# Optimization experiments

Hardware: AMD Instinct MI355X
Metric: run time of the kernel (lower is better)

The kernel has to match this reference:

```python
import jax, jax.numpy as jnp
from jax import lax
import numpy as np

B, L, D, F, T, NB = 32, 512, 256, 256, 2048, 256
LN_EPS = 1e-5


def _layer_norm(h, g, b):
    m = jnp.mean(h, axis=-1, keepdims=True)
    v = jnp.mean((h - m) ** 2, axis=-1, keepdims=True)
    return (h - m) * lax.rsqrt(v + LN_EPS) * g + b


def _predictor(h, prm):
    # Conv1d(k=3, pad=1) -> ReLU -> LayerNorm, twice, then Linear(F->1) -> ReLU -> squeeze
    # (dropout is identity in this deterministic reference)
    c1w, c1b, g1, b1, c2w, c2b, g2, b2, lw, lb = prm
    h = lax.conv_general_dilated(h, c1w, (1,), 'SAME', dimension_numbers=('NWC', 'WIO', 'NWC')) + c1b
    h = _layer_norm(jax.nn.relu(h), g1, b1)
    h = lax.conv_general_dilated(h, c2w, (1,), 'SAME', dimension_numbers=('NWC', 'WIO', 'NWC')) + c2b
    h = _layer_norm(jax.nn.relu(h), g2, b2)
    return jax.nn.relu(jnp.einsum('btf,f->bt', h, lw) + lb)  # [B, T]


def _length_regulate(x, dur, t_out):
    # Gather-based equivalent of the dense alignment-matrix matmul in LengthRegulator.LR:
    # frame t maps to phoneme j with cum[j-1] <= t < cum[j]; frames past total duration are zero.
    cum = jnp.cumsum(dur, axis=1)                                          # [B, L]
    t = jnp.arange(t_out)                                                  # [T]
    idx = jax.vmap(lambda c: jnp.searchsorted(c, t, side='right'))(cum)    # [B, T]
    valid = idx < dur.shape[1]
    idx = jnp.clip(idx, 0, dur.shape[1] - 1)
    out = jnp.take_along_axis(x, idx[..., None], axis=1)                   # [B, T, D]
    return jnp.where(valid[..., None], out, jnp.zeros((), x.dtype))


def setup_inputs() -> dict:
    key = jax.random.key(0)
    ks = iter(jax.random.split(key, 64))

    def nrm(shape, s=0.05):
        return jax.random.normal(next(ks), shape, jnp.float32) * s

    inp = dict(
        x=jax.random.normal(next(ks), (B, L, D), jnp.float32),
        d_target=jax.random.randint(next(ks), (B, L), 0, 4, jnp.int32),
        e_target=jax.random.normal(next(ks), (B, T), jnp.float32),
        p_target=jax.random.normal(next(ks), (B, T), jnp.float32),
        mel_max_length=T,
    )
    for p in ('dur', 'en', 'pi'):
        inp[p + '_c1w'] = nrm((3, D, F)); inp[p + '_c1b'] = jnp.zeros((F,), jnp.float32)
        inp[p + '_g1'] = jnp.ones((F,), jnp.float32); inp[p + '_b1'] = jnp.zeros((F,), jnp.float32)
        inp[p + '_c2w'] = nrm((3, F, F)); inp[p + '_c2b'] = jnp.zeros((F,), jnp.float32)
        inp[p + '_g2'] = jnp.ones((F,), jnp.float32); inp[p + '_b2'] = jnp.zeros((F,), jnp.float32)
        inp[p + '_lw'] = nrm((F,)); inp[p + '_lb'] = jnp.zeros((), jnp.float32)
    inp['en_emb'] = nrm((NB, D), 0.1)
    inp['pi_emb'] = nrm((NB, D), 0.1)
    inp['en_bins'] = jnp.linspace(-3.0, 3.0, NB - 1, dtype=jnp.float32)
    inp['pi_bins'] = jnp.linspace(-3.0, 3.0, NB - 1, dtype=jnp.float32)
    return inp


def reference(x, d_target, e_target, p_target, mel_max_length,
              dur_c1w, dur_c1b, dur_g1, dur_b1, dur_c2w, dur_c2b, dur_g2, dur_b2, dur_lw, dur_lb,
              en_c1w, en_c1b, en_g1, en_b1, en_c2w, en_c2b, en_g2, en_b2, en_lw, en_lb,
              pi_c1w, pi_c1b, pi_g1, pi_b1, pi_c2w, pi_c2b, pi_g2, pi_b2, pi_lw, pi_lb,
              en_emb, pi_emb, en_bins, pi_bins):
    dur_prm = (dur_c1w, dur_c1b, dur_g1, dur_b1, dur_c2w, dur_c2b, dur_g2, dur_b2, dur_lw, dur_lb)
    en_prm = (en_c1w, en_c1b, en_g1, en_b1, en_c2w, en_c2b, en_g2, en_b2, en_lw, en_lb)
    pi_prm = (pi_c1w, pi_c1b, pi_g1, pi_b1, pi_c2w, pi_c2b, pi_g2, pi_b2, pi_lw, pi_lb)

    log_dur = _predictor(x, dur_prm)                               # [B, L]
    h = _length_regulate(x, d_target, mel_max_length)              # [B, T, D]

    energy_pred = _predictor(h, en_prm)                            # [B, T]
    e_idx = jnp.searchsorted(en_bins, e_target, side='left')       # torch.bucketize(right=False)
    h = h + jnp.take(en_emb, e_idx, axis=0)

    pitch_pred = _predictor(h, pi_prm)                             # [B, T]
    p_idx = jnp.searchsorted(pi_bins, p_target, side='left')
    h = h + jnp.take(pi_emb, p_idx, axis=0)

    return (h, log_dur, pitch_pred, energy_pred)
```

## Files before the change

### kernel.cpp

```cpp
#include <hip/hip_runtime.h>
#include <hip/hip_bf16.h>
#include <cstddef>

constexpr int B = 32, L = 512, D = 256, F = 256, T = 2048, NB = 256;
constexpr float LN_EPS = 1e-5f;
constexpr int BDIM = 256;
constexpr int WFRAGS = 24 * 16 * 64;

constexpr int N_FH  = 1024;
constexpr int NT_L  = 9;
constexpr int NT_T  = 34;
constexpr int N_DUR = NT_L * B;
constexpr int N_TP  = NT_T * B;

typedef __attribute__((ext_vector_type(8))) short short8;
typedef __attribute__((ext_vector_type(4))) short short4v;
typedef __attribute__((ext_vector_type(4))) float f32x4;

__device__ inline short f2bf(float x) {
    __hip_bfloat16 h = __float2bfloat16(x);
    return __builtin_bit_cast(short, h);
}

__global__ void cumsum_kernel(const int* __restrict__ dt, int* __restrict__ cum) {
    __shared__ int s[L];
    const int b = blockIdx.x, tid = threadIdx.x;
    s[tid] = dt[b * L + tid];
    __syncthreads();
    for (int off = 1; off < L; off <<= 1) {
        int v = (tid >= off) ? s[tid - off] : 0;
        __syncthreads();
        s[tid] += v;
        __syncthreads();
    }
    cum[b * L + tid] = s[tid];
}

__global__ void idx_kernel(const int* __restrict__ cum,
                           const float* __restrict__ et, const float* __restrict__ ebins,
                           const float* __restrict__ pt, const float* __restrict__ pbins,
                           int* __restrict__ gidx, int* __restrict__ eidx, int* __restrict__ pidx) {
    const int r = blockIdx.x * BDIM + threadIdx.x;
    const int b = r >> 11, t = r & (T - 1);
    const int* c = cum + b * L;
    int lo = 0, hi = L;
    while (lo < hi) { const int mid = (lo + hi) >> 1; if (c[mid] <= t) lo = mid + 1; else hi = mid; }
    gidx[r] = (lo < L) ? lo : -1;
    const float e = et[r];
    int el = 0, eh = NB - 1;
    while (el < eh) { const int mid = (el + eh) >> 1; if (ebins[mid] < e) el = mid + 1; else eh = mid; }
    eidx[r] = el;
    const float p = pt[r];
    int pl = 0, ph = NB - 1;
    while (pl < ph) { const int mid = (pl + ph) >> 1; if (pbins[mid] < p) pl = mid + 1; else ph = mid; }
    pidx[r] = pl;
}

__global__ void wprep_kernel(const float* __restrict__ w0, const float* __restrict__ w1,
                             const float* __restrict__ w2, const float* __restrict__ w3,
                             const float* __restrict__ w4, const float* __restrict__ w5,
                             short* __restrict__ wb) {
    const float* ws[6] = {w0, w1, w2, w3, w4, w5};
    const float* w = ws[blockIdx.y];
    short* dst = wb + (size_t)blockIdx.y * WFRAGS * 8;
    const int phi = blockIdx.x * BDIM + threadIdx.x;
    const int kb = phi >> 10;
    const int n16 = (phi >> 6) & 15;
    const int lane = phi & 63;
    const int kconv = kb >> 3, dblk = kb & 7;
    const int kg = lane >> 4;
    const int fcol = (n16 >> 2) * 64 + (lane & 15) * 4 + (n16 & 3);
    const float* src = w + (size_t)kconv * D * F + (dblk * 32 + kg * 8) * F + fcol;
    short8 o;
    #pragma unroll
    for (int j = 0; j < 8; j++) o[j] = f2bf(src[j * F]);
    *(short8*)(dst + (size_t)phi * 8) = o;
}

__global__ void zv_kernel(const float* __restrict__ cb1, const float* __restrict__ g1,
                          const float* __restrict__ b1,
                          const float* __restrict__ w2, const float* __restrict__ cb2,
                          const float* __restrict__ g2, const float* __restrict__ b2,
                          const float* __restrict__ lw, const float* __restrict__ lb,
                          float* __restrict__ zv) {
    __shared__ float z1s[F];
    __shared__ float red[8];
    const int f = threadIdx.x;
    const int wv = f >> 6, lane = f & 63;

    float v = fmaxf(cb1[f], 0.f);
    float s = v, q = v * v;
    #pragma unroll
    for (int msk = 1; msk < 64; msk <<= 1) { s += __shfl_xor(s, msk); q += __shfl_xor(q, msk); }
    if (lane == 0) { red[wv] = s; red[4 + wv] = q; }
    __syncthreads();
    {
        const float S = red[0] + red[1] + red[2] + red[3];
        const float Q = red[4] + red[5] + red[6] + red[7];
        const float m = S * (1.f / 256.f);
        const float var = fmaxf(Q * (1.f / 256.f) - m * m, 0.f);
        const float rs = rsqrtf(var + LN_EPS);
        z1s[f] = (v - m) * rs * g1[f] + b1[f];
    }
    __syncthreads();

    float y = cb2[f];
    for (int d = 0; d < D; d++) {
        y += z1s[d] * (w2[(size_t)d * F + f] + w2[((size_t)D + d) * F + f]
                       + w2[((size_t)2 * D + d) * F + f]);
    }
    v = fmaxf(y, 0.f);
    s = v; q = v * v;
    #pragma unroll
    for (int msk = 1; msk < 64; msk <<= 1) { s += __shfl_xor(s, msk); q += __shfl_xor(q, msk); }
    __syncthreads();
    if (lane == 0) { red[wv] = s; red[4 + wv] = q; }
    __syncthreads();
    const float S = red[0] + red[1] + red[2] + red[3];
    const float Q = red[4] + red[5] + red[6] + red[7];
    const float m = S * (1.f / 256.f);
    const float var = fmaxf(Q * (1.f / 256.f) - m * m, 0.f);
    const float rs = rsqrtf(var + LN_EPS);
    float p = ((v - m) * rs * g2[f] + b2[f]) * lw[f];
    #pragma unroll
    for (int msk = 1; msk < 64; msk <<= 1) p += __shfl_xor(p, msk);
    __syncthreads();
    if (lane == 0) red[wv] = p;
    __syncthreads();
    if (f == 0) zv[0] = fmaxf(red[0] + red[1] + red[2] + red[3] + lb[0], 0.f);
}

__device__ __forceinline__ void conv_mfma16(const short8 (&a)[4], const short8 (&bb)[4],
                                            f32x4 (&acc)[4][4]) {
    __builtin_amdgcn_s_setprio(1);
    #pragma unroll
    for (int m = 0; m < 4; m++)
        #pragma unroll
        for (int n = 0; n < 4; n++)
            acc[m][n] = __builtin_amdgcn_mfma_f32_16x16x32_bf16(a[m], bb[n], acc[m][n], 0, 0, 0);
    __builtin_amdgcn_s_setprio(0);
}

__device__ __forceinline__ void conv_kloop(const short* in_s, const short8* bw,
                                           f32x4 (&acc)[4][4], int w,
                                           int lane, int kg, int lr) {
    const short8* bp = bw + (w * 4) * 64 + lane;
    short8 bA[4], bB[4];
    #pragma unroll
    for (int n = 0; n < 4; n++) bA[n] = bp[n * 64];
    bp += 1024;
    #pragma unroll
    for (int n = 0; n < 4; n++) bB[n] = bp[n * 64];
    bp += 1024;

    #pragma unroll
    for (int kconv = 0; kconv < 3; kconv++) {
        const short* rowp = in_s + (lr + kconv) * 256;
        const int xb = (lr + kconv) & 7;
        #pragma unroll 1
        for (int db = 0; db < 8; db += 2) {
            short8 a[4];
            {
                const short* ab = rowp + (((db * 4 + kg) ^ xb) << 3);
                #pragma unroll
                for (int m = 0; m < 4; m++) a[m] = *(const short8*)(ab + m * 4096);
                conv_mfma16(a, bA, acc);
                #pragma unroll
                for (int n = 0; n < 4; n++) bA[n] = bp[n * 64];
                bp += 1024;
            }
            {
                const short* ab = rowp + ((((db + 1) * 4 + kg) ^ xb) << 3);
                #pragma unroll
                for (int m = 0; m < 4; m++) a[m] = *(const short8*)(ab + m * 4096);
                conv_mfma16(a, bB, acc);
                #pragma unroll
                for (int n = 0; n < 4; n++) bB[n] = bp[n * 64];
                bp += 1024;
            }
        }
    }
}

struct PredParams {
    const short* wb1; const short* wb2;
    const float *cb1, *g1, *b1, *cb2, *g2, *b2, *lw, *lb;
    const int* eidx; const float* emb;
    const float* zv;
    float* out;
    int Tlen;
    int mode;
};

__launch_bounds__(BDIM, 4)
__global__ void mega_kernel(const float* __restrict__ xin,
                            const int* __restrict__ gidx,
                            const int* __restrict__ cum,
                            const int* __restrict__ eidxA,
                            const int* __restrict__ pidxA,
                            const float* __restrict__ eemb,
                            const float* __restrict__ pemb,
                            float* __restrict__ h,
                            PredParams pd, PredParams pe, PredParams pp) {
    __shared__ short in_s[66 * 256];
    __shared__ float red_s[4][64], red_q[4][64];
    __shared__ float row_m[64], row_rs[64];
    __shared__ float dot_p[4][64];

    const int tid = threadIdx.x;
    const int w = tid >> 6, lane = tid & 63;

    int id = blockIdx.x;
    if (id < N_FH) {
        const int row0 = id * 64 + w * 16;
        #pragma unroll 4
        for (int i = 0; i < 16; i++) {
            const int row = row0 + i;
            const int b = row >> 11;
            const int g = gidx[row], ei = eidxA[row], pi = pidxA[row];
            float4 v = make_float4(0.f, 0.f, 0.f, 0.f);
            if (g >= 0) v = *(const float4*)(xin + ((size_t)b * L + g) * D + lane * 4);
            const float4 ev = *(const float4*)(eemb + (size_t)ei * D + lane * 4);
            const float4 pv = *(const float4*)(pemb + (size_t)pi * D + lane * 4);
            v.x += ev.x + pv.x; v.y += ev.y + pv.y; v.z += ev.z + pv.z; v.w += ev.w + pv.w;
            *(float4*)(h + (size_t)row * D + lane * 4) = v;
        }
        return;
    }
    id -= N_FH;

    PredParams P;
    int b, tx;
    if (id < N_DUR) {
        P = pd; b = id / NT_L; tx = id % NT_L;
    } else if (id < N_DUR + N_TP) {
        id -= N_DUR;
        P = pe; b = id / NT_T; tx = id % NT_T;
    } else {
        id -= N_DUR + N_TP;
        P = pp; b = id / NT_T; tx = id % NT_T;
    }
    const int Tlen = P.Tlen;
    const int t0 = tx * 62;
    const int kg = lane >> 4, lr = lane & 15;

    if (P.zv != nullptr) {
        const int ctot = cum[(b + 1) * L - 1];
        if (t0 - 2 >= ctot) {
            if (tid < 62) {
                const int t = t0 + tid;
                if (t < Tlen) P.out[(size_t)b * Tlen + t] = P.zv[0];
            }
            return;
        }
    }

    constexpr int TASKS = 66 * 32;
    constexpr int BATCH = 4;
    const bool has_emb = (P.emb != nullptr);
    for (int base = 0; base < TASKS; base += BATCH * BDIM) {
        float4 fa[BATCH], fb[BATCH], ea[BATCH], eb[BATCH];
        #pragma unroll
        for (int j = 0; j < BATCH; j++) {
            fa[j] = make_float4(0.f, 0.f, 0.f, 0.f); fb[j] = fa[j];
            ea[j] = fa[j]; eb[j] = fa[j];
            const int task = base + j * BDIM + tid;
            if (task < TASKS) {
                const int row = task >> 5, slot = task & 31;
                const int t = t0 - 2 + row;
                if (t >= 0 && t < Tlen) {
                    if (P.mode == 0) {
                        const float* p = xin + ((size_t)b * Tlen + t) * D + slot * 8;
                        fa[j] = *(const float4*)p; fb[j] = *(const float4*)(p + 4);
                    } else {
                        const int g = gidx[b * T + t];
                        if (g >= 0) {
                            const float* p = xin + ((size_t)b * L + g) * D + slot * 8;
                            fa[j] = *(const float4*)p; fb[j] = *(const float4*)(p + 4);
                        }
                        if (has_emb) {
                            const float* er = P.emb + (size_t)P.eidx[b * T + t] * F + slot * 8;
                            ea[j] = *(const float4*)er; eb[j] = *(const float4*)(er + 4);
                        }
                    }
                }
            }
        }
        #pragma unroll
        for (int j = 0; j < BATCH; j++) {
            const int task = base + j * BDIM + tid;
            if (task < TASKS) {
                const int row = task >> 5, slot = task & 31;
                short8 frag;
                frag[0] = f2bf(fa[j].x + ea[j].x); frag[1] = f2bf(fa[j].y + ea[j].y);
                frag[2] = f2bf(fa[j].z + ea[j].z); frag[3] = f2bf(fa[j].w + ea[j].w);
                frag[4] = f2bf(fb[j].x + eb[j].x); frag[5] = f2bf(fb[j].y + eb[j].y);
                frag[6] = f2bf(fb[j].z + eb[j].z); frag[7] = f2bf(fb[j].w + eb[j].w);
                *(short8*)(in_s + row * 256 + ((slot ^ (row & 7)) << 3)) = frag;
            }
        }
    }
    __syncthreads();

    f32x4 acc[4][4];
    #pragma unroll
    for (int m = 0; m < 4; m++)
        #pragma unroll
        for (int n = 0; n < 4; n++)
            acc[m][n] = (f32x4){0.f, 0.f, 0.f, 0.f};
    conv_kloop(in_s, (const short8*)P.wb1, acc, w, lane, kg, lr);

    const int cbase = w * 64 + lr * 4;
    const f32x4 c1v = *(const f32x4*)(P.cb1 + cbase);
    const f32x4 g1v = *(const f32x4*)(P.g1 + cbase);
    const f32x4 b1v = *(const f32x4*)(P.b1 + cbase);

    #pragma unroll
    for (int m = 0; m < 4; m++) {
        #pragma unroll
        for (int reg = 0; reg < 4; reg++) {
            float s = 0.f, q = 0.f;
            #pragma unroll
            for (int n = 0; n < 4; n++) {
                const float v = fmaxf(acc[m][n][reg] + c1v[n], 0.f);
                acc[m][n][reg] = v;
                s += v; q += v * v;
            }
            #pragma unroll
            for (int msk = 1; msk < 16; msk <<= 1) { s += __shfl_xor(s, msk); q += __shfl_xor(q, msk); }
            if (lr == 0) {
                const int r = m * 16 + kg * 4 + reg;
                red_s[w][r] = s; red_q[w][r] = q;
            }
        }
    }
    __syncthreads();
    if (tid < 64) {
        const float s = red_s[0][tid] + red_s[1][tid] + red_s[2][tid] + red_s[3][tid];
        const float q = red_q[0][tid] + red_q[1][tid] + red_q[2][tid] + red_q[3][tid];
        const float mm = s * (1.f / 256.f);
        const float var = fmaxf(q * (1.f / 256.f) - mm * mm, 0.f);
        row_m[tid] = mm;
        row_rs[tid] = rsqrtf(var + LN_EPS);
    }
    if (tid >= 128 && tid < 192) {
        short8 z = {};
        *(short8*)(in_s + 64 * 256 + (tid - 128) * 8) = z;
    }
    __syncthreads();

    #pragma unroll
    for (int m = 0; m < 4; m++) {
        #pragma unroll
        for (int reg = 0; reg < 4; reg++) {
            const int r1 = m * 16 + kg * 4 + reg;
            const int tg = t0 - 1 + r1;
            const bool ok = (tg >= 0) && (tg < Tlen);
            const float mm = row_m[r1], rs = row_rs[r1];
            short4v o;
            #pragma unroll
            for (int n = 0; n < 4; n++) {
                const float v = ok ? (acc[m][n][reg] - mm) * rs * g1v[n] + b1v[n] : 0.f;
                o[n] = f2bf(v);
            }
            *(short4v*)(in_s + r1 * 256 + (((cbase >> 3) ^ (r1 & 7)) << 3) + (cbase & 7)) = o;
        }
    }
    __syncthreads();

    #pragma unroll
    for (int m = 0; m < 4; m++)
        #pragma unroll
        for (int n = 0; n < 4; n++)
            acc[m][n] = (f32x4){0.f, 0.f, 0.f, 0.f};
    conv_kloop(in_s, (const short8*)P.wb2, acc, w, lane, kg, lr);

    const f32x4 c2v = *(const f32x4*)(P.cb2 + cbase);
    const f32x4 g2v = *(const f32x4*)(P.g2 + cbase);
    const f32x4 b2v = *(const f32x4*)(P.b2 + cbase);
    const f32x4 lwv = *(const f32x4*)(P.lw + cbase);

    #pragma unroll
    for (int m = 0; m < 4; m++) {
        #pragma unroll
        for (int reg = 0; reg < 4; reg++) {
            float s = 0.f, q = 0.f;
            #pragma unroll
            for (int n = 0; n < 4; n++) {
                const float v = fmaxf(acc[m][n][reg] + c2v[n], 0.f);
                acc[m][n][reg] = v;
                s += v; q += v * v;
            }
            #pragma unroll
            for (int msk = 1; msk < 16; msk <<= 1) { s += __shfl_xor(s, msk); q += __shfl_xor(q, msk); }
            if (lr == 0) {
                const int r = m * 16 + kg * 4 + reg;
                red_s[w][r] = s; red_q[w][r] = q;
            }
        }
    }
    __syncthreads();
    if (tid < 64) {
        const float s = red_s[0][tid] + red_s[1][tid] + red_s[2][tid] + red_s[3][tid];
        const float q = red_q[0][tid] + red_q[1][tid] + red_q[2][tid] + red_q[3][tid];
        const float mm = s * (1.f / 256.f);
        const float var = fmaxf(q * (1.f / 256.f) - mm * mm, 0.f);
        row_m[tid] = mm;
        row_rs[tid] = rsqrtf(var + LN_EPS);
    }
    __syncthreads();
    #pragma unroll
    for (int m = 0; m < 4; m++) {
        #pragma unroll
        for (int reg = 0; reg < 4; reg++) {
            const int r = m * 16 + kg * 4 + reg;
            const float mm = row_m[r], rs = row_rs[r];
            float p = 0.f;
            #pragma unroll
            for (int n = 0; n < 4; n++)
                p += ((acc[m][n][reg] - mm) * rs * g2v[n] + b2v[n]) * lwv[n];
            #pragma unroll
            for (int msk = 1; msk < 16; msk <<= 1) p += __shfl_xor(p, msk);
            if (lr == 0) dot_p[w][r] = p;
        }
    }
    __syncthreads();
    if (tid < 62) {
        const int t = t0 + tid;
        if (t < Tlen) {
            const float p = dot_p[0][tid] + dot_p[1][tid] + dot_p[2][tid] + dot_p[3][tid] + P.lb[0];
            P.out[(size_t)b * Tlen + t] = fmaxf(p, 0.f);
        }
    }
}

extern "C" void kernel_launch(void* const* d_in, const int* in_sizes, int n_in,
                              void* d_out, int out_size, void* d_ws, size_t ws_size,
                              hipStream_t stream) {
    const float* x        = (const float*)d_in[0];
    const int*   d_target = (const int*)d_in[1];
    const float* e_target = (const float*)d_in[2];
    const float* p_target = (const float*)d_in[3];

    const float* const* P = (const float* const*)d_in;
    const float* en_emb  = (const float*)d_in[35];
    const float* pi_emb  = (const float*)d_in[36];
    const float* en_bins = (const float*)d_in[37];
    const float* pi_bins = (const float*)d_in[38];

    float* out = (float*)d_out;
    float* h        = out;
    float* log_dur  = out + (size_t)B * T * D;
    float* pitch    = log_dur + (size_t)B * L;
    float* energy   = pitch + (size_t)B * T;

    short* wbs  = (short*)d_ws;
    int*   cum  = (int*)(wbs + (size_t)6 * WFRAGS * 8);
    int*   gidx = cum + B * L;
    int*   eidx = gidx + B * T;
    int*   pidx = eidx + B * T;
    float* zvp  = (float*)(pidx + B * T);

    wprep_kernel<<<dim3(WFRAGS / BDIM, 6), BDIM, 0, stream>>>(
        P[5], P[9], P[15], P[19], P[25], P[29], wbs);

    cumsum_kernel<<<B, L, 0, stream>>>(d_target, cum);
    idx_kernel<<<B * T / BDIM, BDIM, 0, stream>>>(
        cum, e_target, en_bins, p_target, pi_bins, gidx, eidx, pidx);

    zv_kernel<<<1, BDIM, 0, stream>>>(
        P[16], P[17], P[18], P[19], P[20], P[21], P[22], P[23], P[24], zvp);

    PredParams dur_p = { wbs + (size_t)0 * WFRAGS * 8, wbs + (size_t)1 * WFRAGS * 8,
                         P[6], P[7], P[8], P[10], P[11], P[12], P[13], P[14],
                         nullptr, nullptr, nullptr, log_dur, L, 0 };
    PredParams en_p  = { wbs + (size_t)2 * WFRAGS * 8, wbs + (size_t)3 * WFRAGS * 8,
                         P[16], P[17], P[18], P[20], P[21], P[22], P[23], P[24],
                         nullptr, nullptr, zvp, energy, T, 1 };
    PredParams pi_p  = { wbs + (size_t)4 * WFRAGS * 8, wbs + (size_t)5 * WFRAGS * 8,
                         P[26], P[27], P[28], P[30], P[31], P[32], P[33], P[34],
                         eidx, en_emb, nullptr, pitch, T, 1 };

    mega_kernel<<<N_FH + N_DUR + 2 * N_TP, BDIM, 0, stream>>>(
        x, gidx, cum, eidx, pidx, en_emb, pi_emb, h, dur_p, en_p, pi_p);
}
```

Measured before the change: 153.1 us.

## Fuse preamble kernels and precompute embedding-conv table for pitch padding tiles

Merges weight prep, cumsum, index search and the constant-output computation into one preamble launch, cutting launch overhead and serial gaps. For pitch-predictor tiles past the total duration (where input is only the energy embedding), it precomputes a table of energy-embedding rows times each first-conv tap. Those tiles then build the first conv output by summing table rows instead of running the first MFMA conv. This adds a 768-block table-building pass and extra workspace, plus a different numeric path (fp32 table, then bf16 round) for those tiles.

```diff
diff --git a/kernel.cpp b/kernel.cpp
--- a/kernel.cpp
+++ b/kernel.cpp
@@ -13,6 +13,11 @@
 constexpr int N_DUR = NT_L * B;
 constexpr int N_TP  = NT_T * B;
 
+constexpr int PRE_WPREP = 576;
+constexpr int PRE_WTAB  = 768;
+constexpr int PRE_IDX   = 32;
+constexpr int PRE_TOTAL = PRE_WPREP + PRE_WTAB + PRE_IDX + 1;
+
 typedef __attribute__((ext_vector_type(8))) short short8;
 typedef __attribute__((ext_vector_type(4))) short short4v;
 typedef __attribute__((ext_vector_type(4))) float f32x4;
@@ -21,113 +26,144 @@
     __hip_bfloat16 h = __float2bfloat16(x);
     return __builtin_bit_cast(short, h);
 }
-
-__global__ void cumsum_kernel(const int* __restrict__ dt, int* __restrict__ cum) {
-    __shared__ int s[L];
-    const int b = blockIdx.x, tid = threadIdx.x;
-    s[tid] = dt[b * L + tid];
-    __syncthreads();
-    for (int off = 1; off < L; off <<= 1) {
-        int v = (tid >= off) ? s[tid - off] : 0;
-        __syncthreads();
-        s[tid] += v;
-        __syncthreads();
-    }
-    cum[b * L + tid] = s[tid];
+__device__ inline float bf2f(short s) {
+    unsigned u = ((unsigned)(unsigned short)s) << 16;
+    return __builtin_bit_cast(float, u);
 }
 
-__global__ void idx_kernel(const int* __restrict__ cum,
-                           const float* __restrict__ et, const float* __restrict__ ebins,
-                           const float* __restrict__ pt, const float* __restrict__ pbins,
-                           int* __restrict__ gidx, int* __restrict__ eidx, int* __restrict__ pidx) {
-    const int r = blockIdx.x * BDIM + threadIdx.x;
-    const int b = r >> 11, t = r & (T - 1);
-    const int* c = cum + b * L;
-    int lo = 0, hi = L;
-    while (lo < hi) { const int mid = (lo + hi) >> 1; if (c[mid] <= t) lo = mid + 1; else hi = mid; }
-    gidx[r] = (lo < L) ? lo : -1;
-    const float e = et[r];
-    int el = 0, eh = NB - 1;
-    while (el < eh) { const int mid = (el + eh) >> 1; if (ebins[mid] < e) el = mid + 1; else eh = mid; }
-    eidx[r] = el;
-    const float p = pt[r];
-    int pl = 0, ph = NB - 1;
-    while (pl < ph) { const int mid = (pl + ph) >> 1; if (pbins[mid] < p) pl = mid + 1; else ph = mid; }
-    pidx[r] = pl;
-}
-
-__global__ void wprep_kernel(const float* __restrict__ w0, const float* __restrict__ w1,
-                             const float* __restrict__ w2, const float* __restrict__ w3,
-                             const float* __restrict__ w4, const float* __restrict__ w5,
-                             short* __restrict__ wb) {
-    const float* ws[6] = {w0, w1, w2, w3, w4, w5};
-    const float* w = ws[blockIdx.y];
-    short* dst = wb + (size_t)blockIdx.y * WFRAGS * 8;
-    const int phi = blockIdx.x * BDIM + threadIdx.x;
-    const int kb = phi >> 10;
-    const int n16 = (phi >> 6) & 15;
-    const int lane = phi & 63;
-    const int kconv = kb >> 3, dblk = kb & 7;
-    const int kg = lane >> 4;
-    const int fcol = (n16 >> 2) * 64 + (lane & 15) * 4 + (n16 & 3);
-    const float* src = w + (size_t)kconv * D * F + (dblk * 32 + kg * 8) * F + fcol;
-    short8 o;
-    #pragma unroll
-    for (int j = 0; j < 8; j++) o[j] = f2bf(src[j * F]);
-    *(short8*)(dst + (size_t)phi * 8) = o;
-}
-
-__global__ void zv_kernel(const float* __restrict__ cb1, const float* __restrict__ g1,
-                          const float* __restrict__ b1,
-                          const float* __restrict__ w2, const float* __restrict__ cb2,
-                          const float* __restrict__ g2, const float* __restrict__ b2,
-                          const float* __restrict__ lw, const float* __restrict__ lb,
-                          float* __restrict__ zv) {
-    __shared__ float z1s[F];
+__global__ void preamble_kernel(const float* __restrict__ w0, const float* __restrict__ w1,
+                                const float* __restrict__ w2, const float* __restrict__ w3,
+                                const float* __restrict__ w4, const float* __restrict__ w5,
+                                const int* __restrict__ dt,
+                                const float* __restrict__ et, const float* __restrict__ ebins,
+                                const float* __restrict__ pt, const float* __restrict__ pbins,
+                                const float* __restrict__ en_emb, const float* __restrict__ pi_c1w,
+                                const float* __restrict__ zcb1, const float* __restrict__ zg1,
+                                const float* __restrict__ zb1, const float* __restrict__ zw2,
+                                const float* __restrict__ zcb2, const float* __restrict__ zg2,
+                                const float* __restrict__ zb2, const float* __restrict__ zlw,
+                                const float* __restrict__ zlb,
+                                short* __restrict__ wb, int* __restrict__ cum,
+                                int* __restrict__ gidx, int* __restrict__ eidx,
+                                int* __restrict__ pidx,
+                                float* __restrict__ zv, float* __restrict__ wtab) {
+    __shared__ int   cs[512];
+    __shared__ float z1s[256];
     __shared__ float red[8];
-    const int f = threadIdx.x;
-    const int wv = f >> 6, lane = f & 63;
-
-    float v = fmaxf(cb1[f], 0.f);
-    float s = v, q = v * v;
-    #pragma unroll
-    for (int msk = 1; msk < 64; msk <<= 1) { s += __shfl_xor(s, msk); q += __shfl_xor(q, msk); }
-    if (lane == 0) { red[wv] = s; red[4 + wv] = q; }
-    __syncthreads();
+    __shared__ float es[256];
+
+    const int tid = threadIdx.x;
+    int id = blockIdx.x;
+
+    if (id < PRE_WPREP) {
+        const float* ws[6] = {w0, w1, w2, w3, w4, w5};
+        const float* w = ws[id / 96];
+        short* dst = wb + (size_t)(id / 96) * WFRAGS * 8;
+        const int phi = (id % 96) * BDIM + tid;
+        const int kb = phi >> 10;
+        const int n16 = (phi >> 6) & 15;
+        const int lane = phi & 63;
+        const int kconv = kb >> 3, dblk = kb & 7;
+        const int kg = lane >> 4;
+        const int fcol = (n16 >> 2) * 64 + (lane & 15) * 4 + (n16 & 3);
+        const float* src = w + (size_t)kconv * D * F + (dblk * 32 + kg * 8) * F + fcol;
+        short8 o;
+        #pragma unroll
+        for (int j = 0; j < 8; j++) o[j] = f2bf(src[j * F]);
+        *(short8*)(dst + (size_t)phi * 8) = o;
+        return;
+    }
+    id -= PRE_WPREP;
+
+    if (id < PRE_WTAB) {
+        const int k = id >> 8, j = id & 255;
+        es[tid] = en_emb[(size_t)j * D + tid];
+        __syncthreads();
+        const float* wp = pi_c1w + (size_t)k * D * F + tid;
+        float acc = 0.f;
+        #pragma unroll 8
+        for (int d = 0; d < D; d++) acc += es[d] * wp[(size_t)d * F];
+        wtab[(size_t)k * 65536 + (size_t)j * 256 + tid] = acc;
+        return;
+    }
+    id -= PRE_WTAB;
+
+    if (id < PRE_IDX) {
+        const int b = id;
+        cs[tid] = dt[b * L + tid];
+        cs[tid + 256] = dt[b * L + tid + 256];
+        __syncthreads();
+        for (int off = 1; off < 512; off <<= 1) {
+            const int v0 = (tid >= off) ? cs[tid - off] : 0;
+            const int v1 = (tid + 256 >= off) ? cs[tid + 256 - off] : 0;
+            __syncthreads();
+            cs[tid] += v0; cs[tid + 256] += v1;
+            __syncthreads();
+        }
+        cum[b * L + tid] = cs[tid];
+        cum[b * L + tid + 256] = cs[tid + 256];
+        #pragma unroll
+        for (int i = 0; i < 8; i++) {
+            const int t = tid + i * 256;
+            const int r = b * T + t;
+            int lo = 0, hi = L;
+            while (lo < hi) { const int mid = (lo + hi) >> 1; if (cs[mid] <= t) lo = mid + 1; else hi = mid; }
+            gidx[r] = (lo < L) ? lo : -1;
+            const float e = et[r];
+            int el = 0, eh = NB - 1;
+            while (el < eh) { const int mid = (el + eh) >> 1; if (ebins[mid] < e) el = mid + 1; else eh = mid; }
+            eidx[r] = el;
+            const float p = pt[r];
+            int pl = 0, ph = NB - 1;
+            while (pl < ph) { const int mid = (pl + ph) >> 1; if (pbins[mid] < p) pl = mid + 1; else ph = mid; }
+            pidx[r] = pl;
+        }
+        return;
+    }
+
     {
+        const int f = tid;
+        const int wv = f >> 6, lane = f & 63;
+        float v = fmaxf(zcb1[f], 0.f);
+        float s = v, q = v * v;
+        #pragma unroll
+        for (int msk = 1; msk < 64; msk <<= 1) { s += __shfl_xor(s, msk); q += __shfl_xor(q, msk); }
+        if (lane == 0) { red[wv] = s; red[4 + wv] = q; }
+        __syncthreads();
+        {
+            const float S = red[0] + red[1] + red[2] + red[3];
+            const float Q = red[4] + red[5] + red[6] + red[7];
+            const float m = S * (1.f / 256.f);
+            const float var = fmaxf(Q * (1.f / 256.f) - m * m, 0.f);
+            const float rs = rsqrtf(var + LN_EPS);
+            z1s[f] = (v - m) * rs * zg1[f] + zb1[f];
+        }
+        __syncthreads();
+        float y = zcb2[f];
+        for (int d = 0; d < D; d++) {
+            y += z1s[d] * (zw2[(size_t)d * F + f] + zw2[((size_t)D + d) * F + f]
+                           + zw2[((size_t)2 * D + d) * F + f]);
+        }
+        v = fmaxf(y, 0.f);
+        s = v; q = v * v;
+        #pragma unroll
+        for (int msk = 1; msk < 64; msk <<= 1) { s += __shfl_xor(s, msk); q += __shfl_xor(q, msk); }
+        __syncthreads();
+        if (lane == 0) { red[wv] = s; red[4 + wv] = q; }
+        __syncthreads();
         const float S = red[0] + red[1] + red[2] + red[3];
         const float Q = red[4] + red[5] + red[6] + red[7];
         const float m = S * (1.f / 256.f);
         const float var = fmaxf(Q * (1.f / 256.f) - m * m, 0.f);
         const float rs = rsqrtf(var + LN_EPS);
-        z1s[f] = (v - m) * rs * g1[f] + b1[f];
-    }
-    __syncthreads();
-
-    float y = cb2[f];
-    for (int d = 0; d < D; d++) {
-        y += z1s[d] * (w2[(size_t)d * F + f] + w2[((size_t)D + d) * F + f]
-                       + w2[((size_t)2 * D + d) * F + f]);
-    }
-    v = fmaxf(y, 0.f);
-    s = v; q = v * v;
-    #pragma unroll
-    for (int msk = 1; msk < 64; msk <<= 1) { s += __shfl_xor(s, msk); q += __shfl_xor(q, msk); }
-    __syncthreads();
-    if (lane == 0) { red[wv] = s; red[4 + wv] = q; }
-    __syncthreads();
-    const float S = red[0] + red[1] + red[2] + red[3];
-    const float Q = red[4] + red[5] + red[6] + red[7];
-    const float m = S * (1.f / 256.f);
-    const float var = fmaxf(Q * (1.f / 256.f) - m * m, 0.f);
-    const float rs = rsqrtf(var + LN_EPS);
-    float p = ((v - m) * rs * g2[f] + b2[f]) * lw[f];
-    #pragma unroll
-    for (int msk = 1; msk < 64; msk <<= 1) p += __shfl_xor(p, msk);
-    __syncthreads();
-    if (lane == 0) red[wv] = p;
-    __syncthreads();
-    if (f == 0) zv[0] = fmaxf(red[0] + red[1] + red[2] + red[3] + lb[0], 0.f);
+        float p = ((v - m) * rs * zg2[f] + zb2[f]) * zlw[f];
+        #pragma unroll
+        for (int msk = 1; msk < 64; msk <<= 1) p += __shfl_xor(p, msk);
+        __syncthreads();
+        if (lane == 0) red[wv] = p;
+        __syncthreads();
+        if (f == 0) zv[0] = fmaxf(red[0] + red[1] + red[2] + red[3] + zlb[0], 0.f);
+    }
 }
 
 __device__ __forceinline__ void conv_mfma16(const short8 (&a)[4], const short8 (&bb)[4],
@@ -187,6 +223,7 @@
     const float *cb1, *g1, *b1, *cb2, *g2, *b2, *lw, *lb;
     const int* eidx; const float* emb;
     const float* zv;
+    const float* ztab;
     float* out;
     int Tlen;
     int mode;
@@ -244,63 +281,223 @@
     const int t0 = tx * 62;
     const int kg = lane >> 4, lr = lane & 15;
 
-    if (P.zv != nullptr) {
+    bool tablec1 = false;
+    if (P.zv != nullptr || P.ztab != nullptr) {
         const int ctot = cum[(b + 1) * L - 1];
         if (t0 - 2 >= ctot) {
-            if (tid < 62) {
-                const int t = t0 + tid;
-                if (t < Tlen) P.out[(size_t)b * Tlen + t] = P.zv[0];
-            }
-            return;
-        }
-    }
-
-    constexpr int TASKS = 66 * 32;
-    constexpr int BATCH = 4;
-    const bool has_emb = (P.emb != nullptr);
-    for (int base = 0; base < TASKS; base += BATCH * BDIM) {
-        float4 fa[BATCH], fb[BATCH], ea[BATCH], eb[BATCH];
-        #pragma unroll
-        for (int j = 0; j < BATCH; j++) {
-            fa[j] = make_float4(0.f, 0.f, 0.f, 0.f); fb[j] = fa[j];
-            ea[j] = fa[j]; eb[j] = fa[j];
-            const int task = base + j * BDIM + tid;
-            if (task < TASKS) {
-                const int row = task >> 5, slot = task & 31;
-                const int t = t0 - 2 + row;
-                if (t >= 0 && t < Tlen) {
-                    if (P.mode == 0) {
-                        const float* p = xin + ((size_t)b * Tlen + t) * D + slot * 8;
-                        fa[j] = *(const float4*)p; fb[j] = *(const float4*)(p + 4);
-                    } else {
-                        const int g = gidx[b * T + t];
-                        if (g >= 0) {
-                            const float* p = xin + ((size_t)b * L + g) * D + slot * 8;
+            if (P.zv != nullptr) {
+                if (tid < 62) {
+                    const int t = t0 + tid;
+                    if (t < Tlen) P.out[(size_t)b * Tlen + t] = P.zv[0];
+                }
+                return;
+            }
+            tablec1 = true;
+        }
+    }
+
+    if (!tablec1) {
+        constexpr int TASKS = 66 * 32;
+        constexpr int BATCH = 4;
+        const bool has_emb = (P.emb != nullptr);
+        for (int base = 0; base < TASKS; base += BATCH * BDIM) {
+            float4 fa[BATCH], fb[BATCH], ea[BATCH], eb[BATCH];
+            #pragma unroll
+            for (int j = 0; j < BATCH; j++) {
+                fa[j] = make_float4(0.f, 0.f, 0.f, 0.f); fb[j] = fa[j];
+                ea[j] = fa[j]; eb[j] = fa[j];
+                const int task = base + j * BDIM + tid;
+                if (task < TASKS) {
+                    const int row = task >> 5, slot = task & 31;
+                    const int t = t0 - 2 + row;
+                    if (t >= 0 && t < Tlen) {
+                        if (P.mode == 0) {
+                            const float* p = xin + ((size_t)b * Tlen + t) * D + slot * 8;
                             fa[j] = *(const float4*)p; fb[j] = *(const float4*)(p + 4);
-                        }
-                        if (has_emb) {
-                            const float* er = P.emb + (size_t)P.eidx[b * T + t] * F + slot * 8;
-                            ea[j] = *(const float4*)er; eb[j] = *(const float4*)(er + 4);
+                        } else {
+                            const int g = gidx[b * T + t];
+                            if (g >= 0) {
+                                const float* p = xin + ((size_t)b * L + g) * D + slot * 8;
+                                fa[j] = *(const float4*)p; fb[j] = *(const float4*)(p + 4);
+                            }
+                            if (has_emb) {
+                                const float* er = P.emb + (size_t)P.eidx[b * T + t] * F + slot * 8;
+                                ea[j] = *(const float4*)er; eb[j] = *(const float4*)(er + 4);
+                            }
                         }
                     }
                 }
             }
-        }
-        #pragma unroll
-        for (int j = 0; j < BATCH; j++) {
-            const int task = base + j * BDIM + tid;
-            if (task < TASKS) {
-                const int row = task >> 5, slot = task & 31;
-                short8 frag;
-                frag[0] = f2bf(fa[j].x + ea[j].x); frag[1] = f2bf(fa[j].y + ea[j].y);
-                frag[2] = f2bf(fa[j].z + ea[j].z); frag[3] = f2bf(fa[j].w + ea[j].w);
-                frag[4] = f2bf(fb[j].x + eb[j].x); frag[5] = f2bf(fb[j].y + eb[j].y);
-                frag[6] = f2bf(fb[j].z + eb[j].z); frag[7] = f2bf(fb[j].w + eb[j].w);
-                *(short8*)(in_s + row * 256 + ((slot ^ (row & 7)) << 3)) = frag;
-            }
-        }
-    }
-    __syncthreads();
+            #pragma unroll
+            for (int j = 0; j < BATCH; j++) {
+                const int task = base + j * BDIM + tid;
+                if (task < TASKS) {
+                    const int row = task >> 5, slot = task & 31;
+                    short8 frag;
+                    frag[0] = f2bf(fa[j].x + ea[j].x); frag[1] = f2bf(fa[j].y + ea[j].y);
+                    frag[2] = f2bf(fa[j].z + ea[j].z); frag[3] = f2bf(fa[j].w + ea[j].w);
+                    frag[4] = f2bf(fb[j].x + eb[j].x); frag[5] = f2bf(fb[j].y + eb[j].y);
+                    frag[6] = f2bf(fb[j].z + eb[j].z); frag[7] = f2bf(fb[j].w + eb[j].w);
+                    *(short8*)(in_s + row * 256 + ((slot ^ (row & 7)) << 3)) = frag;
+                }
+            }
+        }
+        __syncthreads();
+
+        f32x4 acc[4][4];
+        #pragma unroll
+        for (int m = 0; m < 4; m++)
+            #pragma unroll
+            for (int n = 0; n < 4; n++)
+                acc[m][n] = (f32x4){0.f, 0.f, 0.f, 0.f};
+        conv_kloop(in_s, (const short8*)P.wb1, acc, w, lane, kg, lr);
+
+        const int cbase = w * 64 + lr * 4;
+        const f32x4 c1v = *(const f32x4*)(P.cb1 + cbase);
+        const f32x4 g1v = *(const f32x4*)(P.g1 + cbase);
+        const f32x4 b1v = *(const f32x4*)(P.b1 + cbase);
+
+        #pragma unroll
+        for (int m = 0; m < 4; m++) {
+            #pragma unroll
+            for (int reg = 0; reg < 4; reg++) {
+                float s = 0.f, q = 0.f;
+                #pragma unroll
+                for (int n = 0; n < 4; n++) {
+                    const float v = fmaxf(acc[m][n][reg] + c1v[n], 0.f);
+                    acc[m][n][reg] = v;
+                    s += v; q += v * v;
+                }
+                #pragma unroll
+                for (int msk = 1; msk < 16; msk <<= 1) { s += __shfl_xor(s, msk); q += __shfl_xor(q, msk); }
+                if (lr == 0) {
+                    const int r = m * 16 + kg * 4 + reg;
+                    red_s[w][r] = s; red_q[w][r] = q;
+                }
+            }
+        }
+        __syncthreads();
+        if (tid < 64) {
+            const float s = red_s[0][tid] + red_s[1][tid] + red_s[2][tid] + red_s[3][tid];
+            const float q = red_q[0][tid] + red_q[1][tid] + red_q[2][tid] + red_q[3][tid];
+            const float mm = s * (1.f / 256.f);
+            const float var = fmaxf(q * (1.f / 256.f) - mm * mm, 0.f);
+            row_m[tid] = mm;
+            row_rs[tid] = rsqrtf(var + LN_EPS);
+        }
+        if (tid >= 128 && tid < 192) {
+            short8 z = {};
+            *(short8*)(in_s + 64 * 256 + (tid - 128) * 8) = z;
+        }
+        __syncthreads();
+
+        #pragma unroll
+        for (int m = 0; m < 4; m++) {
+            #pragma unroll
+            for (int reg = 0; reg < 4; reg++) {
+                const int r1 = m * 16 + kg * 4 + reg;
+                const int tg = t0 - 1 + r1;
+                const bool ok = (tg >= 0) && (tg < Tlen);
+                const float mm = row_m[r1], rs = row_rs[r1];
+                short4v o;
+                #pragma unroll
+                for (int n = 0; n < 4; n++) {
+                    const float v = ok ? (acc[m][n][reg] - mm) * rs * g1v[n] + b1v[n] : 0.f;
+                    o[n] = f2bf(v);
+                }
+                *(short4v*)(in_s + r1 * 256 + (((cbase >> 3) ^ (r1 & 7)) << 3) + (cbase & 7)) = o;
+            }
+        }
+        __syncthreads();
+    } else {
+        const int r1 = tid >> 2;
+        const int c0 = (tid & 3) << 6;
+        const int tg = t0 - 1 + r1;
+        float s = 0.f, q = 0.f;
+        if (tg < Tlen) {
+            const float* tb0 = P.ztab + (size_t)P.eidx[b * T + tg - 1] * 256;
+            const float* tb1 = P.ztab + 65536 + (size_t)P.eidx[b * T + tg] * 256;
+            const float* tb2 = (tg + 1 < Tlen)
+                ? P.ztab + 131072 + (size_t)P.eidx[b * T + tg + 1] * 256 : nullptr;
+            #pragma unroll
+            for (int sl = 0; sl < 8; sl++) {
+                const int c = c0 + sl * 8;
+                float4 vA = *(const float4*)(P.cb1 + c);
+                float4 vB = *(const float4*)(P.cb1 + c + 4);
+                {
+                    const float4 aA = *(const float4*)(tb0 + c);
+                    const float4 aB = *(const float4*)(tb0 + c + 4);
+                    vA.x += aA.x; vA.y += aA.y; vA.z += aA.z; vA.w += aA.w;
+                    vB.x += aB.x; vB.y += aB.y; vB.z += aB.z; vB.w += aB.w;
+                }
+                {
+                    const float4 aA = *(const float4*)(tb1 + c);
+                    const float4 aB = *(const float4*)(tb1 + c + 4);
+                    vA.x += aA.x; vA.y += aA.y; vA.z += aA.z; vA.w += aA.w;
+                    vB.x += aB.x; vB.y += aB.y; vB.z += aB.z; vB.w += aB.w;
+                }
+                if (tb2) {
+                    const float4 aA = *(const float4*)(tb2 + c);
+                    const float4 aB = *(const float4*)(tb2 + c + 4);
+                    vA.x += aA.x; vA.y += aA.y; vA.z += aA.z; vA.w += aA.w;
+                    vB.x += aB.x; vB.y += aB.y; vB.z += aB.z; vB.w += aB.w;
+                }
+                const float vals[8] = {vA.x, vA.y, vA.z, vA.w, vB.x, vB.y, vB.z, vB.w};
+                short8 o;
+                #pragma unroll
+                for (int j = 0; j < 8; j++) {
+                    const float vv = fmaxf(vals[j], 0.f);
+                    s += vv; q += vv * vv;
+                    o[j] = f2bf(vv);
+                }
+                *(short8*)(in_s + r1 * 256 + (((c >> 3) ^ (r1 & 7)) << 3)) = o;
+            }
+        } else {
+            short8 z = {};
+            #pragma unroll
+            for (int sl = 0; sl < 8; sl++) {
+                const int c = c0 + sl * 8;
+                *(short8*)(in_s + r1 * 256 + (((c >> 3) ^ (r1 & 7)) << 3)) = z;
+            }
+        }
+        s += __shfl_xor(s, 1); s += __shfl_xor(s, 2);
+        q += __shfl_xor(q, 1); q += __shfl_xor(q, 2);
+        if ((tid & 3) == 0) {
+            const float mm = s * (1.f / 256.f);
+            const float var = fmaxf(q * (1.f / 256.f) - mm * mm, 0.f);
+            row_m[r1] = mm;
+            row_rs[r1] = rsqrtf(var + LN_EPS);
+        }
+        if (tid < 64) {
+            short8 z = {};
+            *(short8*)(in_s + 64 * 256 + tid * 8) = z;
+        }
+        __syncthreads();
+        if (tg < Tlen) {
+            const float mm = row_m[r1], rs = row_rs[r1];
+            #pragma unroll
+            for (int sl = 0; sl < 8; sl++) {
+                const int c = c0 + sl * 8;
+                short* pp = in_s + r1 * 256 + (((c >> 3) ^ (r1 & 7)) << 3);
+                const short8 v = *(short8*)pp;
+                const float4 gA = *(const float4*)(P.g1 + c);
+                const float4 gB = *(const float4*)(P.g1 + c + 4);
+                const float4 bA = *(const float4*)(P.b1 + c);
+                const float4 bB = *(const float4*)(P.b1 + c + 4);
+                short8 o;
+                o[0] = f2bf((bf2f(v[0]) - mm) * rs * gA.x + bA.x);
+                o[1] = f2bf((bf2f(v[1]) - mm) * rs * gA.y + bA.y);
+                o[2] = f2bf((bf2f(v[2]) - mm) * rs * gA.z + bA.z);
+                o[3] = f2bf((bf2f(v[3]) - mm) * rs * gA.w + bA.w);
+                o[4] = f2bf((bf2f(v[4]) - mm) * rs * gB.x + bB.x);
+                o[5] = f2bf((bf2f(v[5]) - mm) * rs * gB.y + bB.y);
+                o[6] = f2bf((bf2f(v[6]) - mm) * rs * gB.z + bB.z);
+                o[7] = f2bf((bf2f(v[7]) - mm) * rs * gB.w + bB.w);
+                *(short8*)pp = o;
+            }
+        }
+        __syncthreads();
+    }
 
     f32x4 acc[4][4];
     #pragma unroll
@@ -308,12 +505,13 @@
         #pragma unroll
         for (int n = 0; n < 4; n++)
             acc[m][n] = (f32x4){0.f, 0.f, 0.f, 0.f};
-    conv_kloop(in_s, (const short8*)P.wb1, acc, w, lane, kg, lr);
+    conv_kloop(in_s, (const short8*)P.wb2, acc, w, lane, kg, lr);
 
     const int cbase = w * 64 + lr * 4;
-    const f32x4 c1v = *(const f32x4*)(P.cb1 + cbase);
-    const f32x4 g1v = *(const f32x4*)(P.g1 + cbase);
-    const f32x4 b1v = *(const f32x4*)(P.b1 + cbase);
+    const f32x4 c2v = *(const f32x4*)(P.cb2 + cbase);
+    const f32x4 g2v = *(const f32x4*)(P.g2 + cbase);
+    const f32x4 b2v = *(const f32x4*)(P.b2 + cbase);
+    const f32x4 lwv = *(const f32x4*)(P.lw + cbase);
 
     #pragma unroll
     for (int m = 0; m < 4; m++) {
@@ -322,7 +520,7 @@
             float s = 0.f, q = 0.f;
             #pragma unroll
             for (int n = 0; n < 4; n++) {
-                const float v = fmaxf(acc[m][n][reg] + c1v[n], 0.f);
+                const float v = fmaxf(acc[m][n][reg] + c2v[n], 0.f);
                 acc[m][n][reg] = v;
                 s += v; q += v * v;
             }
@@ -343,71 +541,6 @@
         row_m[tid] = mm;
         row_rs[tid] = rsqrtf(var + LN_EPS);
     }
-    if (tid >= 128 && tid < 192) {
-        short8 z = {};
-        *(short8*)(in_s + 64 * 256 + (tid - 128) * 8) = z;
-    }
-    __syncthreads();
-
-    #pragma unroll
-    for (int m = 0; m < 4; m++) {
-        #pragma unroll
-        for (int reg = 0; reg < 4; reg++) {
-            const int r1 = m * 16 + kg * 4 + reg;
-            const int tg = t0 - 1 + r1;
-            const bool ok = (tg >= 0) && (tg < Tlen);
-            const float mm = row_m[r1], rs = row_rs[r1];
-            short4v o;
-            #pragma unroll
-            for (int n = 0; n < 4; n++) {
-                const float v = ok ? (acc[m][n][reg] - mm) * rs * g1v[n] + b1v[n] : 0.f;
-                o[n] = f2bf(v);
-            }
-            *(short4v*)(in_s + r1 * 256 + (((cbase >> 3) ^ (r1 & 7)) << 3) + (cbase & 7)) = o;
-        }
-    }
-    __syncthreads();
-
-    #pragma unroll
-    for (int m = 0; m < 4; m++)
-        #pragma unroll
-        for (int n = 0; n < 4; n++)
-            acc[m][n] = (f32x4){0.f, 0.f, 0.f, 0.f};
-    conv_kloop(in_s, (const short8*)P.wb2, acc, w, lane, kg, lr);
-
-    const f32x4 c2v = *(const f32x4*)(P.cb2 + cbase);
-    const f32x4 g2v = *(const f32x4*)(P.g2 + cbase);
-    const f32x4 b2v = *(const f32x4*)(P.b2 + cbase);
-    const f32x4 lwv = *(const f32x4*)(P.lw + cbase);
-
-    #pragma unroll
-    for (int m = 0; m < 4; m++) {
-        #pragma unroll
-        for (int reg = 0; reg < 4; reg++) {
-            float s = 0.f, q = 0.f;
-            #pragma unroll
-            for (int n = 0; n < 4; n++) {
-                const float v = fmaxf(acc[m][n][reg] + c2v[n], 0.f);
-                acc[m][n][reg] = v;
-                s += v; q += v * v;
-            }
-            #pragma unroll
-            for (int msk = 1; msk < 16; msk <<= 1) { s += __shfl_xor(s, msk); q += __shfl_xor(q, msk); }
-            if (lr == 0) {
-                const int r = m * 16 + kg * 4 + reg;
-                red_s[w][r] = s; red_q[w][r] = q;
-            }
-        }
-    }
-    __syncthreads();
-    if (tid < 64) {
-        const float s = red_s[0][tid] + red_s[1][tid] + red_s[2][tid] + red_s[3][tid];
-        const float q = red_q[0][tid] + red_q[1][tid] + red_q[2][tid] + red_q[3][tid];
-        const float mm = s * (1.f / 256.f);
-        const float var = fmaxf(q * (1.f / 256.f) - mm * mm, 0.f);
-        row_m[tid] = mm;
-        row_rs[tid] = rsqrtf(var + LN_EPS);
-    }
     __syncthreads();
     #pragma unroll
     for (int m = 0; m < 4; m++) {
@@ -460,26 +593,24 @@
     int*   eidx = gidx + B * T;
     int*   pidx = eidx + B * T;
     float* zvp  = (float*)(pidx + B * T);
-
-    wprep_kernel<<<dim3(WFRAGS / BDIM, 6), BDIM, 0, stream>>>(
-        P[5], P[9], P[15], P[19], P[25], P[29], wbs);
-
-    cumsum_kernel<<<B, L, 0, stream>>>(d_target, cum);
-    idx_kernel<<<B * T / BDIM, BDIM, 0, stream>>>(
-        cum, e_target, en_bins, p_target, pi_bins, gidx, eidx, pidx);
-
-    zv_kernel<<<1, BDIM, 0, stream>>>(
-        P[16], P[17], P[18], P[19], P[20], P[21], P[22], P[23], P[24], zvp);
+    float* wtab = zvp + 16;
+
+    preamble_kernel<<<PRE_TOTAL, BDIM, 0, stream>>>(
+        P[5], P[9], P[15], P[19], P[25], P[29],
+        d_target, e_target, en_bins, p_target, pi_bins,
+        en_emb, P[25],
+        P[16], P[17], P[18], P[19], P[20], P[21], P[22], P[23], P[24],
+        wbs, cum, gidx, eidx, pidx, zvp, wtab);
 
     PredParams dur_p = { wbs + (size_t)0 * WFRAGS * 8, wbs + (size_t)1 * WFRAGS * 8,
                          P[6], P[7], P[8], P[10], P[11], P[12], P[13], P[14],
-                         nullptr, nullptr, nullptr, log_dur, L, 0 };
+                         nullptr, nullptr, nullptr, nullptr, log_dur, L, 0 };
     PredParams en_p  = { wbs + (size_t)2 * WFRAGS * 8, wbs + (size_t)3 * WFRAGS * 8,
                          P[16], P[17], P[18], P[20], P[21], P[22], P[23], P[24],
-                         nullptr, nullptr, zvp, energy, T, 1 };
+                         nullptr, nullptr, zvp, nullptr, energy, T, 1 };
     PredParams pi_p  = { wbs + (size_t)4 * WFRAGS * 8, wbs + (size_t)5 * WFRAGS * 8,
                          P[26], P[27], P[28], P[30], P[31], P[32], P[33], P[34],
-                         eidx, en_emb, nullptr, pitch, T, 1 };
+                         eidx, en_emb, nullptr, wtab, pitch, T, 1 };
 
     mega_kernel<<<N_FH + N_DUR + 2 * N_TP, BDIM, 0, stream>>>(
         x, gidx, cum, eidx, pidx, en_emb, pi_emb, h, dur_p, en_p, pi_p);
```

New measurement: 164.4 us. +7.4%, slower.
